# Performance work log

Hardware: AMD Instinct MI355X
Metric: run time of the kernel (lower is better)

The kernel has to match this reference:

```python
import jax, jax.numpy as jnp
import numpy as np

N_DOCS, DOC_LEN, H = 10000, 200, 128   # document token vectors [N, d, h]
B, QLEN, NPIDS = 16, 32, 500           # batch, query tokens, candidate pids per query
TOPK = 100


def setup_inputs() -> dict:
    key = jax.random.key(0)
    k1, k2, k3 = jax.random.split(key, 3)
    q_vectors = jax.random.normal(k1, (B, QLEN, H), dtype=jnp.float32)
    vectors = jax.random.normal(k2, (N_DOCS, DOC_LEN, H), dtype=jnp.float32)
    pids = jax.random.randint(k3, (B, NPIDS), 0, N_DOCS, dtype=jnp.int32)
    boundaries = jnp.array([0, N_DOCS], dtype=jnp.int32)
    return {"q_vectors": q_vectors, "pids": pids, "vectors": vectors,
            "boundaries": boundaries, "k": TOPK}


def _dedupe_row(row):
    # torch.unique-like: sort ascending, replace duplicate entries with -1.
    # (Original pads each row's unique set with -1; only tie-order in the
    #  downstream top-k can differ, the score/pid sets are identical.)
    s = jnp.sort(row)
    dup = jnp.concatenate([jnp.zeros((1,), dtype=bool), s[1:] == s[:-1]])
    return jnp.where(dup, jnp.int32(-1), s)


def reference(q_vectors, pids, vectors, boundaries, k):
    lo = boundaries[0]
    n_vec = vectors.shape[0]
    pids = pids - lo
    pids = jnp.where((pids < 0) | (pids >= n_vec), jnp.int32(-1), pids)
    pids = jax.vmap(_dedupe_row)(pids)                       # [b, K]

    # gather doc token vectors (pid == -1 wraps to last doc; masked below,
    # matching torch's vectors[pids] semantics for -1)
    d_vectors = vectors[pids]                                # [b, K, d, h]
    scores = jnp.einsum('bqh,bkdh->bkqd', q_vectors, d_vectors)
    scores = scores.max(axis=-1).sum(axis=-1)                # MaxSim: max over doc tokens, sum over query tokens -> [b, K]
    scores = jnp.where(pids < 0, -jnp.inf, scores)

    top_scores, top_idx = jax.lax.top_k(scores, k)           # sorted descending
    top_pids = jnp.take_along_axis(pids, top_idx, axis=-1)
    top_pids = jnp.where(top_pids >= 0, top_pids + lo, top_pids)
    return top_scores, top_pids
```

## Files before the change

### kernel.cpp

```cpp
#include <hip/hip_runtime.h>
#include <float.h>
#include <limits.h>

#define NB     16
#define QLEN   32
#define HDIM   128
#define NPIDS  500
#define NDOCS  10000
#define DLEN   200
#define TOPK   100
#define VROW   (DLEN * HDIM)

typedef __bf16 bf16x8 __attribute__((ext_vector_type(8)));
typedef float  f32x16 __attribute__((ext_vector_type(16)));

__global__ __launch_bounds__(512) void dedupe_kernel(const int* __restrict__ pids,
                                                     const int* __restrict__ boundaries,
                                                     int* __restrict__ dpids) {
    __shared__ int s[512];
    const int b = blockIdx.x;
    const int t = threadIdx.x;
    const int lo = boundaries[0];

    int v = INT_MAX;
    if (t < NPIDS) {
        int p = pids[b * NPIDS + t] - lo;
        if (p < 0 || p >= NDOCS) p = -1;
        v = p;
    }
    s[t] = v;
    __syncthreads();

    for (int k = 2; k <= 512; k <<= 1) {
        for (int j = k >> 1; j > 0; j >>= 1) {
            int ixj = t ^ j;
            if (ixj > t) {
                int a = s[t], c = s[ixj];
                bool up = ((t & k) == 0);
                if ((a > c) == up) { s[t] = c; s[ixj] = a; }
            }
            __syncthreads();
        }
    }

    if (t < NPIDS) {
        int val = s[t];
        int o = val;
        if (val == INT_MAX) o = -1;
        else if (t > 0 && val == s[t - 1]) o = -1;
        dpids[b * NPIDS + t] = o;
    }
}

__device__ __forceinline__ void split3(float a, __bf16& h, __bf16& m, __bf16& l) {
    h = (__bf16)a;
    float r1 = a - (float)h;
    m = (__bf16)r1;
    float r2 = r1 - (float)m;
    l = (__bf16)r2;
}

__device__ __forceinline__ void split3_pack8(const float4 c0, const float4 c1,
                                             bf16x8& H, bf16x8& M, bf16x8& L) {
    float f[8] = {c0.x, c0.y, c0.z, c0.w, c1.x, c1.y, c1.z, c1.w};
    bf16x8 Ht, Mt, Lt;
    #pragma unroll
    for (int j = 0; j < 8; ++j) {
        __bf16 hh, mm, ll;
        split3(f[j], hh, mm, ll);
        Ht[j] = hh; Mt[j] = mm; Lt[j] = ll;
    }
    H = Ht; M = Mt; L = Lt;
}

__global__ __launch_bounds__(256, 2) void score_kernel(const float* __restrict__ qv,
                                                       const float* __restrict__ vectors,
                                                       const int* __restrict__ dpids,
                                                       float* __restrict__ scores) {
    const int t    = threadIdx.x;
    const int w    = t >> 6;
    const int lane = t & 63;
    const int row  = lane & 31;
    const int half = lane >> 5;

    const int cbase = (blockIdx.x * 4 + w) * 2;
    const int b     = cbase / NPIDS;

    bf16x8 qh[8], qm[8], ql[8];
    {
        const float* qb = qv + ((size_t)b * QLEN + row) * HDIM + half * 8;
        #pragma unroll
        for (int ks = 0; ks < 8; ++ks) {
            const float4 a0 = *(const float4*)(qb + ks * 16);
            const float4 a1 = *(const float4*)(qb + ks * 16 + 4);
            split3_pack8(a0, a1, qh[ks], qm[ks], ql[ks]);
        }
    }

    for (int ci = 0; ci < 2; ++ci) {
        const int c   = cbase + ci;
        const int pid = dpids[c];
        if (pid < 0) {
            if (lane == 0) scores[c] = -__builtin_inff();
            continue;
        }

        const float* vb = vectors + (size_t)pid * VROW + half * 8;

        float rmax[16];
        #pragma unroll
        for (int j = 0; j < 16; ++j) rmax[j] = -FLT_MAX;

        const float* vt0 = vb + (size_t)row * HDIM;
        float4 pf[4][2];
        #pragma unroll
        for (int s = 0; s < 4; ++s) {
            pf[s][0] = *(const float4*)(vt0 + s * 16);
            pf[s][1] = *(const float4*)(vt0 + s * 16 + 4);
        }

        #pragma unroll 1
        for (int tile = 0; tile < 7; ++tile) {
            int tok = tile * 32 + row;
            if (tok > DLEN - 1) tok = DLEN - 1;
            const float* vt = vb + (size_t)tok * HDIM;
            int tokn = (tile + 1) * 32 + row;
            if (tokn > DLEN - 1) tokn = DLEN - 1;
            const float* vtn = vb + (size_t)tokn * HDIM;

            f32x16 acc;
            #pragma unroll
            for (int j = 0; j < 16; ++j) acc[j] = 0.0f;

            #pragma unroll
            for (int ks = 0; ks < 8; ++ks) {
                const int slot = ks & 3;
                const float4 c0 = pf[slot][0];
                const float4 c1 = pf[slot][1];

                if (ks < 4) {
                    pf[slot][0] = *(const float4*)(vt + (ks + 4) * 16);
                    pf[slot][1] = *(const float4*)(vt + (ks + 4) * 16 + 4);
                } else if (tile < 6) {
                    pf[slot][0] = *(const float4*)(vtn + (ks - 4) * 16);
                    pf[slot][1] = *(const float4*)(vtn + (ks - 4) * 16 + 4);
                }

                bf16x8 vh, vm, vl;
                split3_pack8(c0, c1, vh, vm, vl);
                acc = __builtin_amdgcn_mfma_f32_32x32x16_bf16(qh[ks], vh, acc, 0, 0, 0);
                acc = __builtin_amdgcn_mfma_f32_32x32x16_bf16(qh[ks], vm, acc, 0, 0, 0);
                acc = __builtin_amdgcn_mfma_f32_32x32x16_bf16(qm[ks], vh, acc, 0, 0, 0);
                acc = __builtin_amdgcn_mfma_f32_32x32x16_bf16(qh[ks], vl, acc, 0, 0, 0);
                acc = __builtin_amdgcn_mfma_f32_32x32x16_bf16(ql[ks], vh, acc, 0, 0, 0);
            }

            #pragma unroll
            for (int j = 0; j < 16; ++j) rmax[j] = fmaxf(rmax[j], acc[j]);
        }

        double dsum = 0.0;
        #pragma unroll
        for (int j = 0; j < 16; ++j) {
            float m = rmax[j];
            m = fmaxf(m, __shfl_xor(m, 1));
            m = fmaxf(m, __shfl_xor(m, 2));
            m = fmaxf(m, __shfl_xor(m, 4));
            m = fmaxf(m, __shfl_xor(m, 8));
            m = fmaxf(m, __shfl_xor(m, 16));
            dsum += (double)m;
        }
        dsum += __shfl_xor(dsum, 32);
        if (lane == 0) scores[c] = (float)dsum;
    }
}

__global__ __launch_bounds__(512) void topk_kernel(const float* __restrict__ scores,
                                                   const int* __restrict__ dpids,
                                                   const int* __restrict__ boundaries,
                                                   float* __restrict__ out) {
    __shared__ float ss[512];
    __shared__ int   sp[512];
    const int b = blockIdx.x;
    const int t = threadIdx.x;
    const int lo = boundaries[0];

    float sc = -__builtin_inff();
    int   p  = -1;
    if (t < NPIDS) {
        p = dpids[b * NPIDS + t];
        sc = (p < 0) ? -__builtin_inff() : scores[b * NPIDS + t];
    }
    ss[t] = sc;
    sp[t] = p;
    __syncthreads();

    for (int k = 2; k <= 512; k <<= 1) {
        for (int j = k >> 1; j > 0; j >>= 1) {
            int ixj = t ^ j;
            if (ixj > t) {
                float a = ss[t], c = ss[ixj];
                bool down = ((t & k) == 0);
                bool swap = down ? (a < c) : (a > c);
                if (swap) {
                    int pa = sp[t], pc = sp[ixj];
                    ss[t] = c;   ss[ixj] = a;
                    sp[t] = pc;  sp[ixj] = pa;
                }
            }
            __syncthreads();
        }
    }

    if (t < TOPK) {
        out[b * TOPK + t] = ss[t];
        int pp = sp[t];
        out[NB * TOPK + b * TOPK + t] = (pp >= 0) ? (float)(pp + lo) : -1.0f;
    }
}

extern "C" void kernel_launch(void* const* d_in, const int* in_sizes, int n_in,
                              void* d_out, int out_size, void* d_ws, size_t ws_size,
                              hipStream_t stream) {
    const float* qv        = (const float*)d_in[0];
    const int*   pids      = (const int*)d_in[1];
    const float* vectors   = (const float*)d_in[2];
    const int*   boundaries= (const int*)d_in[3];

    int*   dpids  = (int*)d_ws;
    float* scores = (float*)((char*)d_ws + 32768);

    dedupe_kernel<<<NB, 512, 0, stream>>>(pids, boundaries, dpids);
    score_kernel <<<(NB * NPIDS) / 8, 256, 0, stream>>>(qv, vectors, dpids, scores);
    topk_kernel  <<<NB, 512, 0, stream>>>(scores, dpids, boundaries, (float*)d_out);
}
```

Measured before the change: 163.9 us.

## Stage split query fragments in LDS to cut registers and raise occupancy

The bf16 hi/mid/lo split of the query is now computed once per block by one wave and stored in shared memory, instead of being held in 24 vector registers in every wave. Each MFMA step reloads the fragments from LDS, which frees registers so launch bounds can ask for 3 blocks per CU. The grid becomes 2D with one batch per y-row, and the last block of each row clamps its candidate start, so some candidates are scored twice. The trade is extra LDS reads inside the inner loop and a block barrier, in exchange for more waves to hide global loads.

```diff
diff --git a/kernel.cpp b/kernel.cpp
--- a/kernel.cpp
+++ b/kernel.cpp
@@ -73,7 +73,7 @@
     H = Ht; M = Mt; L = Lt;
 }
 
-__global__ __launch_bounds__(256, 2) void score_kernel(const float* __restrict__ qv,
+__global__ __launch_bounds__(256, 3) void score_kernel(const float* __restrict__ qv,
                                                        const float* __restrict__ vectors,
                                                        const int* __restrict__ dpids,
                                                        float* __restrict__ scores) {
@@ -82,20 +82,28 @@
     const int lane = t & 63;
     const int row  = lane & 31;
     const int half = lane >> 5;
-
-    const int cbase = (blockIdx.x * 4 + w) * 2;
-    const int b     = cbase / NPIDS;
-
-    bf16x8 qh[8], qm[8], ql[8];
-    {
+    const int b    = blockIdx.y;
+
+    int cs = blockIdx.x * 8 + w * 2;
+    if (cs > NPIDS - 2) cs = NPIDS - 2;
+    const int cbase = b * NPIDS + cs;
+
+    __shared__ __align__(16) unsigned char qlds[8][3][64][16];
+
+    if (t < 64) {
         const float* qb = qv + ((size_t)b * QLEN + row) * HDIM + half * 8;
         #pragma unroll
         for (int ks = 0; ks < 8; ++ks) {
             const float4 a0 = *(const float4*)(qb + ks * 16);
             const float4 a1 = *(const float4*)(qb + ks * 16 + 4);
-            split3_pack8(a0, a1, qh[ks], qm[ks], ql[ks]);
-        }
-    }
+            bf16x8 H, M, L;
+            split3_pack8(a0, a1, H, M, L);
+            *(bf16x8*)qlds[ks][0][t] = H;
+            *(bf16x8*)qlds[ks][1][t] = M;
+            *(bf16x8*)qlds[ks][2][t] = L;
+        }
+    }
+    __syncthreads();
 
     for (int ci = 0; ci < 2; ++ci) {
         const int c   = cbase + ci;
@@ -148,11 +156,16 @@
 
                 bf16x8 vh, vm, vl;
                 split3_pack8(c0, c1, vh, vm, vl);
-                acc = __builtin_amdgcn_mfma_f32_32x32x16_bf16(qh[ks], vh, acc, 0, 0, 0);
-                acc = __builtin_amdgcn_mfma_f32_32x32x16_bf16(qh[ks], vm, acc, 0, 0, 0);
-                acc = __builtin_amdgcn_mfma_f32_32x32x16_bf16(qm[ks], vh, acc, 0, 0, 0);
-                acc = __builtin_amdgcn_mfma_f32_32x32x16_bf16(qh[ks], vl, acc, 0, 0, 0);
-                acc = __builtin_amdgcn_mfma_f32_32x32x16_bf16(ql[ks], vh, acc, 0, 0, 0);
+
+                const bf16x8 qh = *(const bf16x8*)qlds[ks][0][lane];
+                const bf16x8 qm = *(const bf16x8*)qlds[ks][1][lane];
+                const bf16x8 ql = *(const bf16x8*)qlds[ks][2][lane];
+
+                acc = __builtin_amdgcn_mfma_f32_32x32x16_bf16(qh, vh, acc, 0, 0, 0);
+                acc = __builtin_amdgcn_mfma_f32_32x32x16_bf16(qh, vm, acc, 0, 0, 0);
+                acc = __builtin_amdgcn_mfma_f32_32x32x16_bf16(qm, vh, acc, 0, 0, 0);
+                acc = __builtin_amdgcn_mfma_f32_32x32x16_bf16(qh, vl, acc, 0, 0, 0);
+                acc = __builtin_amdgcn_mfma_f32_32x32x16_bf16(ql, vh, acc, 0, 0, 0);
             }
 
             #pragma unroll
@@ -231,6 +244,7 @@
     float* scores = (float*)((char*)d_ws + 32768);
 
     dedupe_kernel<<<NB, 512, 0, stream>>>(pids, boundaries, dpids);
-    score_kernel <<<(NB * NPIDS) / 8, 256, 0, stream>>>(qv, vectors, dpids, scores);
+    dim3 sgrid((NPIDS + 7) / 8, NB);
+    score_kernel <<<sgrid, 256, 0, stream>>>(qv, vectors, dpids, scores);
     topk_kernel  <<<NB, 512, 0, stream>>>(scores, dpids, boundaries, (float*)d_out);
 }
```

After: 309.6 us. 88.9% more time.
